# Kernel tuning notes

Hardware: AMD Instinct MI355X
Metric: run time of the kernel (lower is better)

The kernel has to match this reference:

```python
import jax, jax.numpy as jnp
import numpy as np


def setup_inputs() -> dict:
    key = jax.random.key(0)
    ks = jax.random.split(key, 12)
    M, B, N, FD, BD, BVD, H = 4096, 8, 512, 128, 128, 6, 64
    return {
        "f_pre_in": jax.random.normal(ks[0], (M, FD), jnp.float32),
        "f_pre_batch": jnp.sort(jax.random.randint(ks[1], (M,), 0, B)),
        "b_pre_in": jax.random.normal(ks[2], (B, BD, N), jnp.float32),
        "bv_in": jax.random.normal(ks[3], (B, BVD, N), jnp.float32),
        "Wf": jax.random.normal(ks[4], (H, FD), jnp.float32) * 0.05,
        "bf": jax.random.normal(ks[5], (H,), jnp.float32) * 0.05,
        "Wb": jax.random.normal(ks[6], (H, BD), jnp.float32) * 0.05,
        "bb": jax.random.normal(ks[7], (H,), jnp.float32) * 0.05,
        "Wbv": jax.random.normal(ks[8], (H, BVD), jnp.float32) * 0.05,
        "bbv": jax.random.normal(ks[9], (H,), jnp.float32) * 0.05,
        "Wo": jax.random.normal(ks[10], (H, 2 * H), jnp.float32) * 0.05,
        "bo": jax.random.normal(ks[11], (H,), jnp.float32) * 0.05,
    }


def reference(f_pre_in, f_pre_batch, b_pre_in, bv_in, Wf, bf, Wb, bb, Wbv, bbv, Wo, bo):
    # 1x1 Conv1d == channel matmul.
    H = Wf.shape[0]
    h2 = H // 2
    scale = jnp.sqrt(jnp.asarray(H, jnp.float32))  # sqrt(hidden_size)
    f = Wf @ f_pre_in.T + bf[:, None]                                  # (H, M)
    b_feat = jnp.einsum('hd,bdn->bhn', Wb, b_pre_in) + bb[None, :, None]   # (B, H, N)
    bv_feat = jnp.einsum('hc,bcn->bhn', Wbv, bv_in) + bbv[None, :, None]   # (B, H, N)
    # Per-node gather of that node's graph boundary features (f_pre_batch is sorted,
    # so per-node order == torch's per-batch concat order).
    be = b_feat[f_pre_batch, :h2]    # (M, h2, N)
    bg = b_feat[f_pre_batch, h2:]    # (M, h2, N)
    bvg = bv_feat[f_pre_batch]       # (M, H, N)
    # Cross-attention: softmax over the N boundary positions (torch dim=0 of (N, n_b)).
    w_euc = jax.nn.softmax(jnp.einsum('mhn,hm->mn', be, f[:h2]) / scale, axis=-1)  # (M, N)
    w_geo = jax.nn.softmax(jnp.einsum('mhn,hm->mn', bg, f[h2:]) / scale, axis=-1)  # (M, N)
    out_euc = jnp.einsum('mhn,mn->mh', bvg, w_euc)   # (M, H)
    out_geo = jnp.einsum('mhn,mn->mh', bvg, w_geo)   # (M, H)
    cat = jnp.concatenate([out_euc, out_geo], axis=1)  # (M, 2H)
    return cat @ Wo.T + bo                              # (M, H)
```

## Files before the change

kernel.cpp:

```cpp
#include <hip/hip_runtime.h>

#define M_TOT 4096
#define B_TOT 8
#define N_TOT 512
#define FD    128
#define BD    128
#define BVD   6
#define H     64
#define MAX_TILES 264

typedef short short8 __attribute__((ext_vector_type(8)));
typedef float floatx4 __attribute__((ext_vector_type(4)));

__device__ __forceinline__ unsigned short f2bf(float x) {
    union { float f; unsigned int u; } v; v.f = x;
    return (unsigned short)((v.u + 0x7fffu + ((v.u >> 16) & 1u)) >> 16);
}
__device__ __forceinline__ float bf2f(unsigned short u) {
    union { unsigned int u32; float f; } v; v.u32 = ((unsigned int)u) << 16;
    return v.f;
}

__device__ __forceinline__ int lb_dev(const int* __restrict__ arr, int n, int v) {
    int lo = 0, hi = n;
    while (lo < hi) { int mid = (lo + hi) >> 1; if (arr[mid] < v) lo = mid + 1; else hi = mid; }
    return lo;
}

__global__ __launch_bounds__(256) void k_pre(const float* __restrict__ f_pre_in,
                                             const int*   __restrict__ batch,
                                             const float* __restrict__ b_pre_in,
                                             const float* __restrict__ bv_in,
                                             const float* __restrict__ Wf,
                                             const float* __restrict__ bf,
                                             const float* __restrict__ Wb,
                                             const float* __restrict__ bb,
                                             const float* __restrict__ Wbv,
                                             const float* __restrict__ bbv,
                                             const float* __restrict__ Wo,
                                             unsigned short* __restrict__ f_bf,
                                             unsigned short* __restrict__ bFT_bf,
                                             unsigned short* __restrict__ bv_bf,
                                             unsigned short* __restrict__ Wo_bf,
                                             int4*  __restrict__ table) {
    __shared__ __align__(16) char sm[43264];
    const int t = threadIdx.x;
    const int blk = blockIdx.x;

    if (blk < 256) {
        float* fpre = (float*)sm;
        float* WfT  = (float*)(sm + 8448);
        const int m0 = blk * 16;
        for (int i = t; i < 16 * FD; i += 256)
            fpre[(i >> 7) * 132 + (i & 127)] = f_pre_in[(size_t)m0 * FD + i];
        for (int i = t; i < H * FD; i += 256)
            WfT[(i & 127) * 68 + (i >> 7)] = Wf[i];
        __syncthreads();
        const int mi = t >> 4;
        const int h4 = (t & 15) * 4;
        float a0 = bf[h4], a1 = bf[h4 + 1], a2 = bf[h4 + 2], a3 = bf[h4 + 3];
#pragma unroll 4
        for (int d4 = 0; d4 < 32; ++d4) {
            const float4 fp = *(const float4*)&fpre[mi * 132 + d4 * 4];
            const float* fpp = &fp.x;
#pragma unroll
            for (int i = 0; i < 4; ++i) {
                const float4 wv = *(const float4*)&WfT[(d4 * 4 + i) * 68 + h4];
                const float f = fpp[i];
                a0 += f * wv.x; a1 += f * wv.y; a2 += f * wv.z; a3 += f * wv.w;
            }
        }
        ushort4 o; o.x = f2bf(a0); o.y = f2bf(a1); o.z = f2bf(a2); o.w = f2bf(a3);
        *(ushort4*)&f_bf[(size_t)(m0 + mi) * H + h4] = o;
    } else if (blk < 512) {
        float* Wb_l = (float*)sm;
        float* bp   = (float*)(sm + 33024);
        const int idx = blk - 256;
        const int b  = idx >> 5;
        const int n0 = (idx & 31) * 16;
        for (int i = t; i < H * BD; i += 256)
            Wb_l[(i >> 7) * 129 + (i & 127)] = Wb[i];
        for (int i = t; i < BD * 16; i += 256)
            bp[(i >> 4) * 17 + (i & 15)] =
                b_pre_in[(size_t)b * BD * N_TOT + (size_t)(i >> 4) * N_TOT + n0 + (i & 15)];
        __syncthreads();
        const int h  = t & 63;
        const int nl = t >> 6;
        const float bias = bb[h];
        float acc[4] = {bias, bias, bias, bias};
        const float* wr = &Wb_l[h * 129];
#pragma unroll 8
        for (int d = 0; d < BD; ++d) {
            const float w = wr[d];
            acc[0] += w * bp[d * 17 + nl];
            acc[1] += w * bp[d * 17 + nl + 4];
            acc[2] += w * bp[d * 17 + nl + 8];
            acc[3] += w * bp[d * 17 + nl + 12];
        }
#pragma unroll
        for (int j = 0; j < 4; ++j)
            bFT_bf[((size_t)b * N_TOT + n0 + nl + 4 * j) * H + h] = f2bf(acc[j]);
    } else if (blk < 768) {
        const int idx = blk - 512;
        const int b  = idx >> 5;
        const int h  = (idx & 31) * 2 + (t >> 7);
        const int n4 = (t & 127) * 4;
        float w[BVD];
#pragma unroll
        for (int c = 0; c < BVD; ++c) w[c] = Wbv[h * BVD + c];
        const float bias = bbv[h];
        float a0 = bias, a1 = bias, a2 = bias, a3 = bias;
        const float* src = bv_in + (size_t)b * BVD * N_TOT + n4;
#pragma unroll
        for (int c = 0; c < BVD; ++c) {
            const float4 v = *(const float4*)(src + c * N_TOT);
            a0 += w[c] * v.x; a1 += w[c] * v.y; a2 += w[c] * v.z; a3 += w[c] * v.w;
        }
        ushort4 o; o.x = f2bf(a0); o.y = f2bf(a1); o.z = f2bf(a2); o.w = f2bf(a3);
        *(ushort4*)&bv_bf[((size_t)b * H + h) * N_TOT + n4] = o;
    } else {
        int starts[9];
#pragma unroll
        for (int b = 0; b <= 8; ++b) starts[b] = lb_dev(batch, M_TOT, b);
        int pre[9]; pre[0] = 0;
#pragma unroll
        for (int b = 0; b < 8; ++b) pre[b + 1] = pre[b] + (starts[b + 1] - starts[b] + 15) / 16;
        const int total = pre[8];
        for (int idx = t; idx < MAX_TILES; idx += 256) {
            int4 e = make_int4(0, 0, 0, 0);
            if (idx < total) {
                int b = 0;
                while (pre[b + 1] <= idx) ++b;
                const int r0 = starts[b] + (idx - pre[b]) * 16;
                e.x = b; e.y = r0; e.z = min(16, starts[b + 1] - r0);
            }
            table[idx] = e;
        }
        for (int i = t; i < H * 2 * H; i += 256) Wo_bf[i] = f2bf(Wo[i]);
    }
}

__global__ __launch_bounds__(256) void k_main(const unsigned short* __restrict__ f_bf,
                                              const unsigned short* __restrict__ bFT_bf,
                                              const unsigned short* __restrict__ bv_bf,
                                              const unsigned short* __restrict__ Wo_bf,
                                              const float* __restrict__ bo,
                                              const int4*  __restrict__ table,
                                              float* __restrict__ out) {
    __shared__ __align__(16) char wreg[4][8704];
    __shared__ __align__(16) float rowsumP[4][2][16];
    __shared__ __align__(16) unsigned short cat_l[16 * 136];

    const int t = threadIdx.x;
    const int wave = t >> 6, l = t & 63, quad = l >> 4, s = l & 15;
    const int4 te = table[blockIdx.x];
    const int b = te.x, m0 = te.y, nr = te.z;
    if (nr == 0) return;

    unsigned short* Wl = (unsigned short*)&wreg[wave][0];
    const floatx4 zero = {0.f, 0.f, 0.f, 0.f};

    const int rclamp = (s < nr) ? s : (nr - 1);
    const unsigned short* fptr = f_bf + (size_t)(m0 + rclamp) * H + quad * 8;
    const short8 fE = *(const short8*)(fptr);
    const short8 fG = *(const short8*)(fptr + 32);
    short8 bvF[4][4];
#pragma unroll
    for (int kc = 0; kc < 4; ++kc)
#pragma unroll
        for (int hc = 0; hc < 4; ++hc)
            bvF[kc][hc] = *(const short8*)(bv_bf +
                ((size_t)b * H + hc * 16 + s) * N_TOT + wave * 128 + kc * 32 + quad * 8);
    short8 woF[4];
#pragma unroll
    for (int kc = 0; kc < 4; ++kc)
        woF[kc] = *(const short8*)(Wo_bf + (size_t)(wave * 16 + s) * 128 + kc * 32 + quad * 8);
    const float bj = bo[wave * 16 + s];

    const unsigned short* bA = bFT_bf + ((size_t)b * N_TOT + wave * 128 + s) * H + quad * 8;
    floatx4 dE[8], dG[8];
#pragma unroll
    for (int c = 0; c < 8; ++c) {
        const short8 aE = *(const short8*)(bA + (size_t)c * 16 * H);
        const short8 aG = *(const short8*)(bA + (size_t)c * 16 * H + 32);
        dE[c] = __builtin_amdgcn_mfma_f32_16x16x32_bf16(aE, fE, zero, 0, 0, 0);
        dG[c] = __builtin_amdgcn_mfma_f32_16x16x32_bf16(aG, fG, zero, 0, 0, 0);
    }

    float rsE = 0.f, rsG = 0.f;
#pragma unroll
    for (int c = 0; c < 8; ++c) {
        ushort4 pE, pG;
        unsigned short u;
        u = f2bf(__expf(dE[c][0] * 0.125f)); rsE += bf2f(u); pE.x = u;
        u = f2bf(__expf(dE[c][1] * 0.125f)); rsE += bf2f(u); pE.y = u;
        u = f2bf(__expf(dE[c][2] * 0.125f)); rsE += bf2f(u); pE.z = u;
        u = f2bf(__expf(dE[c][3] * 0.125f)); rsE += bf2f(u); pE.w = u;
        u = f2bf(__expf(dG[c][0] * 0.125f)); rsG += bf2f(u); pG.x = u;
        u = f2bf(__expf(dG[c][1] * 0.125f)); rsG += bf2f(u); pG.y = u;
        u = f2bf(__expf(dG[c][2] * 0.125f)); rsG += bf2f(u); pG.z = u;
        u = f2bf(__expf(dG[c][3] * 0.125f)); rsG += bf2f(u); pG.w = u;
        *(ushort4*)&Wl[s * 136 + c * 16 + quad * 4]        = pE;
        *(ushort4*)&Wl[2176 + s * 136 + c * 16 + quad * 4] = pG;
    }
    rsE += __shfl_xor(rsE, 16); rsE += __shfl_xor(rsE, 32);
    rsG += __shfl_xor(rsG, 16); rsG += __shfl_xor(rsG, 32);
    if (l < 16) { rowsumP[wave][0][s] = rsE; rowsumP[wave][1][s] = rsG; }

    floatx4 oE[4] = {zero, zero, zero, zero};
    floatx4 oG[4] = {zero, zero, zero, zero};
#pragma unroll
    for (int kc = 0; kc < 4; ++kc) {
        const short8 aE = *(const short8*)&Wl[s * 136 + kc * 32 + quad * 8];
        const short8 aG = *(const short8*)&Wl[2176 + s * 136 + kc * 32 + quad * 8];
#pragma unroll
        for (int hc = 0; hc < 4; ++hc) {
            oE[hc] = __builtin_amdgcn_mfma_f32_16x16x32_bf16(aE, bvF[kc][hc], oE[hc], 0, 0, 0);
            oG[hc] = __builtin_amdgcn_mfma_f32_16x16x32_bf16(aG, bvF[kc][hc], oG[hc], 0, 0, 0);
        }
    }
    {
        float* Op = (float*)&wreg[wave][0];
#pragma unroll
        for (int hc = 0; hc < 4; ++hc) {
            *(floatx4*)&Op[(hc * 16 + s) * 16 + quad * 4]        = oE[hc];
            *(floatx4*)&Op[1024 + (hc * 16 + s) * 16 + quad * 4] = oG[hc];
        }
    }
    __syncthreads();

    {
        const int h  = t >> 2;
        const int r4 = (t & 3) * 4;
        floatx4 sE = zero, sG = zero, rE = zero, rG = zero;
#pragma unroll
        for (int w = 0; w < 4; ++w) {
            const float* opw = (const float*)&wreg[w][0];
            sE += *(const floatx4*)&opw[h * 16 + r4];
            sG += *(const floatx4*)&opw[1024 + h * 16 + r4];
            rE += *(const floatx4*)&rowsumP[w][0][r4];
            rG += *(const floatx4*)&rowsumP[w][1][r4];
        }
#pragma unroll
        for (int i = 0; i < 4; ++i) {
            cat_l[(r4 + i) * 136 + h]      = f2bf(sE[i] / rE[i]);
            cat_l[(r4 + i) * 136 + 64 + h] = f2bf(sG[i] / rG[i]);
        }
    }
    __syncthreads();

    {
        floatx4 acc = zero;
#pragma unroll
        for (int kc = 0; kc < 4; ++kc) {
            const short8 aC = *(const short8*)&cat_l[s * 136 + kc * 32 + quad * 8];
            acc = __builtin_amdgcn_mfma_f32_16x16x32_bf16(aC, woF[kc], acc, 0, 0, 0);
        }
        const int j = wave * 16 + s;
#pragma unroll
        for (int reg = 0; reg < 4; ++reg) {
            const int r = quad * 4 + reg;
            if (r < nr) out[(size_t)(m0 + r) * H + j] = acc[reg] + bj;
        }
    }
}

extern "C" void kernel_launch(void* const* d_in, const int* in_sizes, int n_in,
                              void* d_out, int out_size, void* d_ws, size_t ws_size,
                              hipStream_t stream) {
    const float* f_pre_in = (const float*)d_in[0];
    const int*   f_batch  = (const int*)  d_in[1];
    const float* b_pre_in = (const float*)d_in[2];
    const float* bv_in    = (const float*)d_in[3];
    const float* Wf       = (const float*)d_in[4];
    const float* bf       = (const float*)d_in[5];
    const float* Wb       = (const float*)d_in[6];
    const float* bb       = (const float*)d_in[7];
    const float* Wbv      = (const float*)d_in[8];
    const float* bbv      = (const float*)d_in[9];
    const float* Wo       = (const float*)d_in[10];
    const float* bo       = (const float*)d_in[11];
    float* out = (float*)d_out;

    unsigned short* f_bf   = (unsigned short*)d_ws;
    unsigned short* bFT_bf = f_bf + (size_t)M_TOT * H;
    unsigned short* bv_bf  = bFT_bf + (size_t)B_TOT * N_TOT * H;
    unsigned short* Wo_bf  = bv_bf + (size_t)B_TOT * H * N_TOT;
    int4* table = (int4*)(Wo_bf + (size_t)H * 2 * H);

    k_pre <<<769, 256, 0, stream>>>(f_pre_in, f_batch, b_pre_in, bv_in,
                                    Wf, bf, Wb, bb, Wbv, bbv, Wo,
                                    f_bf, bFT_bf, bv_bf, Wo_bf, table);
    k_main<<<MAX_TILES, 256, 0, stream>>>(f_bf, bFT_bf, bv_bf, Wo_bf, bo, table, out);
}
```

Before: 109.4 us.

## Split euclidean and geodesic attention branches across separate waves in k_main

The main kernel now launches 512 threads per block instead of 256. Waves 0-3 handle the euclidean half of the attention and waves 4-7 the geodesic half, each covering a quarter of the N positions. Each wave keeps half the accumulators and issues half the MFMAs, which raises parallelism per tile and should cut register pressure. In exchange, every bv fragment is loaded twice per block, and the final output projection is restricted to the first four waves.

```diff
diff --git a/kernel.cpp b/kernel.cpp
--- a/kernel.cpp
+++ b/kernel.cpp
@@ -140,19 +140,21 @@
     }
 }
 
-__global__ __launch_bounds__(256) void k_main(const unsigned short* __restrict__ f_bf,
+__global__ __launch_bounds__(512) void k_main(const unsigned short* __restrict__ f_bf,
                                               const unsigned short* __restrict__ bFT_bf,
                                               const unsigned short* __restrict__ bv_bf,
                                               const unsigned short* __restrict__ Wo_bf,
                                               const float* __restrict__ bo,
                                               const int4*  __restrict__ table,
                                               float* __restrict__ out) {
-    __shared__ __align__(16) char wreg[4][8704];
-    __shared__ __align__(16) float rowsumP[4][2][16];
+    __shared__ __align__(16) char wreg[8][4352];
+    __shared__ __align__(16) float rowsumP[8][16];
     __shared__ __align__(16) unsigned short cat_l[16 * 136];
 
     const int t = threadIdx.x;
     const int wave = t >> 6, l = t & 63, quad = l >> 4, s = l & 15;
+    const int eg = wave >> 2;
+    const int nq = wave & 3;
     const int4 te = table[blockIdx.x];
     const int b = te.x, m0 = te.y, nr = te.z;
     if (nr == 0) return;
@@ -161,95 +163,76 @@
     const floatx4 zero = {0.f, 0.f, 0.f, 0.f};
 
     const int rclamp = (s < nr) ? s : (nr - 1);
-    const unsigned short* fptr = f_bf + (size_t)(m0 + rclamp) * H + quad * 8;
-    const short8 fE = *(const short8*)(fptr);
-    const short8 fG = *(const short8*)(fptr + 32);
+    const short8 fX = *(const short8*)(f_bf + (size_t)(m0 + rclamp) * H + eg * 32 + quad * 8);
     short8 bvF[4][4];
 #pragma unroll
     for (int kc = 0; kc < 4; ++kc)
 #pragma unroll
         for (int hc = 0; hc < 4; ++hc)
             bvF[kc][hc] = *(const short8*)(bv_bf +
-                ((size_t)b * H + hc * 16 + s) * N_TOT + wave * 128 + kc * 32 + quad * 8);
+                ((size_t)b * H + hc * 16 + s) * N_TOT + nq * 128 + kc * 32 + quad * 8);
     short8 woF[4];
 #pragma unroll
     for (int kc = 0; kc < 4; ++kc)
-        woF[kc] = *(const short8*)(Wo_bf + (size_t)(wave * 16 + s) * 128 + kc * 32 + quad * 8);
-    const float bj = bo[wave * 16 + s];
-
-    const unsigned short* bA = bFT_bf + ((size_t)b * N_TOT + wave * 128 + s) * H + quad * 8;
-    floatx4 dE[8], dG[8];
+        woF[kc] = *(const short8*)(Wo_bf + (size_t)((wave & 3) * 16 + s) * 128 + kc * 32 + quad * 8);
+    const float bj = bo[(wave & 3) * 16 + s];
+
+    const unsigned short* bA = bFT_bf + ((size_t)b * N_TOT + nq * 128 + s) * H + eg * 32 + quad * 8;
+    floatx4 d[8];
 #pragma unroll
     for (int c = 0; c < 8; ++c) {
-        const short8 aE = *(const short8*)(bA + (size_t)c * 16 * H);
-        const short8 aG = *(const short8*)(bA + (size_t)c * 16 * H + 32);
-        dE[c] = __builtin_amdgcn_mfma_f32_16x16x32_bf16(aE, fE, zero, 0, 0, 0);
-        dG[c] = __builtin_amdgcn_mfma_f32_16x16x32_bf16(aG, fG, zero, 0, 0, 0);
-    }
-
-    float rsE = 0.f, rsG = 0.f;
+        const short8 aX = *(const short8*)(bA + (size_t)c * 16 * H);
+        d[c] = __builtin_amdgcn_mfma_f32_16x16x32_bf16(aX, fX, zero, 0, 0, 0);
+    }
+
+    float rs = 0.f;
 #pragma unroll
     for (int c = 0; c < 8; ++c) {
-        ushort4 pE, pG;
+        ushort4 p;
         unsigned short u;
-        u = f2bf(__expf(dE[c][0] * 0.125f)); rsE += bf2f(u); pE.x = u;
-        u = f2bf(__expf(dE[c][1] * 0.125f)); rsE += bf2f(u); pE.y = u;
-        u = f2bf(__expf(dE[c][2] * 0.125f)); rsE += bf2f(u); pE.z = u;
-        u = f2bf(__expf(dE[c][3] * 0.125f)); rsE += bf2f(u); pE.w = u;
-        u = f2bf(__expf(dG[c][0] * 0.125f)); rsG += bf2f(u); pG.x = u;
-        u = f2bf(__expf(dG[c][1] * 0.125f)); rsG += bf2f(u); pG.y = u;
-        u = f2bf(__expf(dG[c][2] * 0.125f)); rsG += bf2f(u); pG.z = u;
-        u = f2bf(__expf(dG[c][3] * 0.125f)); rsG += bf2f(u); pG.w = u;
-        *(ushort4*)&Wl[s * 136 + c * 16 + quad * 4]        = pE;
-        *(ushort4*)&Wl[2176 + s * 136 + c * 16 + quad * 4] = pG;
-    }
-    rsE += __shfl_xor(rsE, 16); rsE += __shfl_xor(rsE, 32);
-    rsG += __shfl_xor(rsG, 16); rsG += __shfl_xor(rsG, 32);
-    if (l < 16) { rowsumP[wave][0][s] = rsE; rowsumP[wave][1][s] = rsG; }
-
-    floatx4 oE[4] = {zero, zero, zero, zero};
-    floatx4 oG[4] = {zero, zero, zero, zero};
+        u = f2bf(__expf(d[c][0] * 0.125f)); rs += bf2f(u); p.x = u;
+        u = f2bf(__expf(d[c][1] * 0.125f)); rs += bf2f(u); p.y = u;
+        u = f2bf(__expf(d[c][2] * 0.125f)); rs += bf2f(u); p.z = u;
+        u = f2bf(__expf(d[c][3] * 0.125f)); rs += bf2f(u); p.w = u;
+        *(ushort4*)&Wl[s * 136 + c * 16 + quad * 4] = p;
+    }
+    rs += __shfl_xor(rs, 16); rs += __shfl_xor(rs, 32);
+    if (l < 16) rowsumP[wave][s] = rs;
+
+    floatx4 o[4] = {zero, zero, zero, zero};
 #pragma unroll
     for (int kc = 0; kc < 4; ++kc) {
-        const short8 aE = *(const short8*)&Wl[s * 136 + kc * 32 + quad * 8];
-        const short8 aG = *(const short8*)&Wl[2176 + s * 136 + kc * 32 + quad * 8];
-#pragma unroll
-        for (int hc = 0; hc < 4; ++hc) {
-            oE[hc] = __builtin_amdgcn_mfma_f32_16x16x32_bf16(aE, bvF[kc][hc], oE[hc], 0, 0, 0);
-            oG[hc] = __builtin_amdgcn_mfma_f32_16x16x32_bf16(aG, bvF[kc][hc], oG[hc], 0, 0, 0);
-        }
+        const short8 aW = *(const short8*)&Wl[s * 136 + kc * 32 + quad * 8];
+#pragma unroll
+        for (int hc = 0; hc < 4; ++hc)
+            o[hc] = __builtin_amdgcn_mfma_f32_16x16x32_bf16(aW, bvF[kc][hc], o[hc], 0, 0, 0);
     }
     {
         float* Op = (float*)&wreg[wave][0];
 #pragma unroll
-        for (int hc = 0; hc < 4; ++hc) {
-            *(floatx4*)&Op[(hc * 16 + s) * 16 + quad * 4]        = oE[hc];
-            *(floatx4*)&Op[1024 + (hc * 16 + s) * 16 + quad * 4] = oG[hc];
-        }
+        for (int hc = 0; hc < 4; ++hc)
+            *(floatx4*)&Op[(hc * 16 + s) * 16 + quad * 4] = o[hc];
     }
     __syncthreads();
 
     {
-        const int h  = t >> 2;
+        const int h  = t >> 3;
+        const int ge = (t >> 2) & 1;
         const int r4 = (t & 3) * 4;
-        floatx4 sE = zero, sG = zero, rE = zero, rG = zero;
+        floatx4 sm_ = zero, rsum = zero;
 #pragma unroll
         for (int w = 0; w < 4; ++w) {
-            const float* opw = (const float*)&wreg[w][0];
-            sE += *(const floatx4*)&opw[h * 16 + r4];
-            sG += *(const floatx4*)&opw[1024 + h * 16 + r4];
-            rE += *(const floatx4*)&rowsumP[w][0][r4];
-            rG += *(const floatx4*)&rowsumP[w][1][r4];
-        }
-#pragma unroll
-        for (int i = 0; i < 4; ++i) {
-            cat_l[(r4 + i) * 136 + h]      = f2bf(sE[i] / rE[i]);
-            cat_l[(r4 + i) * 136 + 64 + h] = f2bf(sG[i] / rG[i]);
-        }
+            const float* opw = (const float*)&wreg[ge * 4 + w][0];
+            sm_  += *(const floatx4*)&opw[h * 16 + r4];
+            rsum += *(const floatx4*)&rowsumP[ge * 4 + w][r4];
+        }
+#pragma unroll
+        for (int i = 0; i < 4; ++i)
+            cat_l[(r4 + i) * 136 + ge * 64 + h] = f2bf(sm_[i] / rsum[i]);
     }
     __syncthreads();
 
-    {
+    if (wave < 4) {
         floatx4 acc = zero;
 #pragma unroll
         for (int kc = 0; kc < 4; ++kc) {
@@ -291,5 +274,5 @@
     k_pre <<<769, 256, 0, stream>>>(f_pre_in, f_batch, b_pre_in, bv_in,
                                     Wf, bf, Wb, bb, Wbv, bbv, Wo,
                                     f_bf, bFT_bf, bv_bf, Wo_bf, table);
-    k_main<<<MAX_TILES, 256, 0, stream>>>(f_bf, bFT_bf, bv_bf, Wo_bf, bo, table, out);
-}
+    k_main<<<MAX_TILES, 512, 0, stream>>>(f_bf, bFT_bf, bv_bf, Wo_bf, bo, table, out);
+}
```

Result: slower. 115.0 us (+5.1%).
